# Performance work log

Measured on AMD Instinct MI355X. Metric: run time of the kernel, lower is better.

The kernel has to match this reference:

```python
import jax, jax.numpy as jnp
import numpy as np

B, C, H, W, N = 4, 128, 240, 320, 1024
LEVEL = 8.0          # scaling[0] = 4 * img_scale with img_scale=2
E1_LAMDA = 1.0
E2_LAMDA = 2.0 / 7.0
GN_LAMDA = 0.3
EPS = 1e-9


def extract_features(f, coords):
    # f: (B,C,H,W); coords: (B,N,2) float pixel coords as (x, y)
    Bf, Cf, Hf, Wf = f.shape
    x = coords[..., 0]
    y = coords[..., 1]
    x0 = jnp.floor(x)
    y0 = jnp.floor(y)
    wx = (x - x0)[:, None, :]          # (B,1,N)
    wy = (y - y0)[:, None, :]
    x0i = jnp.clip(x0.astype(jnp.int32), 0, Wf - 1)
    x1i = jnp.clip(x0i + 1, 0, Wf - 1)
    y0i = jnp.clip(y0.astype(jnp.int32), 0, Hf - 1)
    y1i = jnp.clip(y0i + 1, 0, Hf - 1)

    def g(fm, yi, xi):                 # fm: (C,H,W), yi/xi: (N,)
        return fm[:, yi, xi]           # (C,N)

    v00 = jax.vmap(g)(f, y0i, x0i)
    v01 = jax.vmap(g)(f, y0i, x1i)
    v10 = jax.vmap(g)(f, y1i, x0i)
    v11 = jax.vmap(g)(f, y1i, x1i)
    out = (v00 * (1 - wx) * (1 - wy) + v01 * wx * (1 - wy)
           + v10 * (1 - wx) * wy + v11 * wx * wy)          # (B,C,N)
    return out.transpose(0, 2, 1).reshape(Bf * coords.shape[1], Cf)


def l2_normalize(f):
    n = jnp.linalg.norm(f, axis=1, keepdims=True)
    return f / jnp.maximum(n, 1e-12)


def torch_gradient(f):
    # central differences with edge replication; gx = d/dx (width), gy = d/dy (height)
    fpx = jnp.pad(f, ((0, 0), (0, 0), (0, 0), (1, 1)), mode='edge')
    fpy = jnp.pad(f, ((0, 0), (0, 0), (1, 1), (0, 0)), mode='edge')
    gx = 0.5 * (fpx[..., 2:] - fpx[..., :-2])
    gy = 0.5 * (fpy[..., 2:, :] - fpy[..., :-2, :])
    return gx, gy


def compute_gn_loss(f_t, fb, ub, noise):
    Bn, Nn, _ = ub.shape
    xs = (2.0 * noise - 1.0) + ub                   # uniform(-1,1) jitter
    f_s = extract_features(fb, xs)
    f_t = l2_normalize(f_t)
    f_s = l2_normalize(f_s)
    r = f_s - f_t                                   # (BN, C)
    gx, gy = torch_gradient(fb)
    Jx = extract_features(gx, xs)                   # (BN, C)
    Jy = extract_features(gy, xs)
    J = jnp.stack([Jx, Jy], axis=-1)                # (BN, C, 2)
    Hm = jnp.einsum('bci,bcj->bij', J, J) + EPS * jnp.eye(2, dtype=J.dtype)
    b = jnp.einsum('bci,bc->bi', J, r)[..., None]   # (BN, 2, 1)
    # closed-form 2x2 inverse
    a = Hm[:, 0, 0]; bb = Hm[:, 0, 1]; c = Hm[:, 1, 0]; d = Hm[:, 1, 1]
    det = a * d - bb * c
    Hinv = jnp.stack([jnp.stack([d, -bb], -1),
                      jnp.stack([-c, a], -1)], -2) / det[:, None, None]
    miu = xs.reshape(Bn * Nn, 2, 1) - Hinv @ b
    diff = (ub.reshape(Bn * Nn, 2, 1) - miu)[..., 0]          # (BN, 2)
    e1 = 0.5 * jnp.sum(jnp.einsum('bi,bij,bj->b', diff, Hm, diff))
    log_det = jnp.log(det)
    e2 = Bn * Nn * jnp.log(jnp.asarray(2.0 * np.pi, dtype=det.dtype)) - 0.5 * jnp.sum(log_det)
    e = E1_LAMDA * e1 + E2_LAMDA * e2
    return e, e1, e2


def setup_inputs() -> dict:
    key = jax.random.key(0)
    k = jax.random.split(key, 7)
    F_a = jax.random.normal(k[0], (B, C, H, W), dtype=jnp.float32)
    F_b = jax.random.normal(k[1], (B, C, H, W), dtype=jnp.float32)
    # full-resolution match coords, safely inside the map after /LEVEL
    xa = jax.random.uniform(k[2], (B, N)) * (W - 5) * LEVEL + 2 * LEVEL
    ya = jax.random.uniform(k[3], (B, N)) * (H - 5) * LEVEL + 2 * LEVEL
    xb = jax.random.uniform(k[4], (B, N)) * (W - 5) * LEVEL + 2 * LEVEL
    yb = jax.random.uniform(k[5], (B, N)) * (H - 5) * LEVEL + 2 * LEVEL
    matches_a = jnp.stack([xa, ya], axis=-1)
    matches_b = jnp.stack([xb, yb], axis=-1)
    noise = jax.random.uniform(k[6], (B, N, 2), dtype=jnp.float32)
    return {"F_a": F_a, "F_b": F_b, "matches_a": matches_a,
            "matches_b": matches_b, "noise": noise}


def reference(F_a, F_b, matches_a, matches_b, noise):
    f_t = extract_features(F_a, matches_a / LEVEL)
    e, e1, e2 = compute_gn_loss(f_t, F_b, matches_b / LEVEL, noise)
    return GN_LAMDA * e, e1, e2
```

## Files before the change

### kernel.cpp

```cpp
#include <hip/hip_runtime.h>
#include <math.h>

#define B_  4
#define C_  128
#define H_  240
#define W_  320
#define N_  1024
#define NPTS (B_ * N_)
#define HW_ (H_ * W_)
#define NBINS 960

typedef float f4 __attribute__((ext_vector_type(4)));
typedef float f2 __attribute__((ext_vector_type(2)));

__device__ __forceinline__ f4 load4(const float* p) {
    f4 v; __builtin_memcpy(&v, p, 16); return v;
}
__device__ __forceinline__ f2 load2(const float* p) {
    f2 v; __builtin_memcpy(&v, p, 8); return v;
}
__device__ __forceinline__ void store2(float* p, f2 v) {
    __builtin_memcpy(p, &v, 8);
}

__global__ __launch_bounds__(1024) void gn_sort_kernel(
    const float* __restrict__ ma, const float* __restrict__ mb,
    const float* __restrict__ noise,
    int* __restrict__ permA, int* __restrict__ permB)
{
    __shared__ int hist[NBINS];
    __shared__ int cursor[NBINS];

    for (int i = threadIdx.x; i < NBINS; i += 1024) hist[i] = 0;
    __syncthreads();
    int keyB[4];
    #pragma unroll
    for (int k = 0; k < 4; ++k) {
        const int p = threadIdx.x + (k << 10);
        const float ys = 2.0f * noise[p * 2 + 1] - 1.0f + mb[p * 2 + 1] * 0.125f;
        const int y0 = min(max((int)floorf(ys), 1), H_ - 3);
        keyB[k] = (p >> 10) * H_ + y0;
        atomicAdd(&hist[keyB[k]], 1);
    }
    __syncthreads();
    if (threadIdx.x < 64) {
        const int lane = threadIdx.x;
        const int base = lane * 15;
        int loc[15]; int s = 0;
        #pragma unroll
        for (int i = 0; i < 15; ++i) { loc[i] = s; s += hist[base + i]; }
        int incl = s;
        #pragma unroll
        for (int off = 1; off < 64; off <<= 1) {
            const int v = __shfl_up(incl, off, 64);
            if (lane >= off) incl += v;
        }
        const int excl = incl - s;
        #pragma unroll
        for (int i = 0; i < 15; ++i) cursor[base + i] = excl + loc[i];
    }
    __syncthreads();
    #pragma unroll
    for (int k = 0; k < 4; ++k) {
        const int p = threadIdx.x + (k << 10);
        permB[atomicAdd(&cursor[keyB[k]], 1)] = p;
    }
    __syncthreads();

    for (int i = threadIdx.x; i < NBINS; i += 1024) hist[i] = 0;
    __syncthreads();
    int keyA[4];
    #pragma unroll
    for (int k = 0; k < 4; ++k) {
        const int p = threadIdx.x + (k << 10);
        const float ya = ma[p * 2 + 1] * 0.125f;
        const int y0 = min(max((int)floorf(ya), 0), H_ - 2);
        keyA[k] = (p >> 10) * H_ + y0;
        atomicAdd(&hist[keyA[k]], 1);
    }
    __syncthreads();
    if (threadIdx.x < 64) {
        const int lane = threadIdx.x;
        const int base = lane * 15;
        int loc[15]; int s = 0;
        #pragma unroll
        for (int i = 0; i < 15; ++i) { loc[i] = s; s += hist[base + i]; }
        int incl = s;
        #pragma unroll
        for (int off = 1; off < 64; off <<= 1) {
            const int v = __shfl_up(incl, off, 64);
            if (lane >= off) incl += v;
        }
        const int excl = incl - s;
        #pragma unroll
        for (int i = 0; i < 15; ++i) cursor[base + i] = excl + loc[i];
    }
    __syncthreads();
    #pragma unroll
    for (int k = 0; k < 4; ++k) {
        const int p = threadIdx.x + (k << 10);
        permA[atomicAdd(&cursor[keyA[k]], 1)] = p;
    }
}

__global__ __launch_bounds__(256) void gn_ft_kernel(
    const float* __restrict__ Fa, const float* __restrict__ ma,
    const int* __restrict__ permA, float* __restrict__ ws_ft)
{
    const int w    = (blockIdx.x << 2) | (threadIdx.x >> 6);
    const int lane = threadIdx.x & 63;
    const int pg   = w >> 6;
    const int c0   = (w & 63) << 1;
    const int p    = permA[(pg << 6) | lane];
    const int b    = p >> 10;

    const float xa = ma[p * 2 + 0] * 0.125f;
    const float ya = ma[p * 2 + 1] * 0.125f;
    const float ax0f = floorf(xa), ay0f = floorf(ya);
    const float awx = xa - ax0f, awy = ya - ay0f;
    const int ax0 = min(max((int)ax0f, 0), W_ - 2);
    const int ay0 = min(max((int)ay0f, 0), H_ - 2);
    const int o0 = ay0 * W_ + ax0;
    const int o1 = o0 + W_;

    const float* __restrict__ fa0 = Fa + ((size_t)(b * C_ + c0)) * HW_;
    const float* __restrict__ fa1 = fa0 + HW_;

    const f2 a0_0 = load2(fa0 + o0);
    const f2 a1_0 = load2(fa0 + o1);
    const f2 a0_1 = load2(fa1 + o0);
    const f2 a1_1 = load2(fa1 + o1);

    const float w00 = (1.f - awx) * (1.f - awy);
    const float w01 = awx * (1.f - awy);
    const float w10 = (1.f - awx) * awy;
    const float w11 = awx * awy;

    f2 ft;
    ft.x = a0_0.x * w00 + a0_0.y * w01 + a1_0.x * w10 + a1_0.y * w11;
    ft.y = a0_1.x * w00 + a0_1.y * w01 + a1_1.x * w10 + a1_1.y * w11;
    store2(ws_ft + (size_t)p * C_ + c0, ft);
}

__global__ __launch_bounds__(256) void gn_fb_kernel(
    const float* __restrict__ Fb, const float* __restrict__ mb,
    const float* __restrict__ noise, const int* __restrict__ permB,
    float* __restrict__ fjp)
{
    const int w    = (blockIdx.x << 2) | (threadIdx.x >> 6);
    const int lane = threadIdx.x & 63;
    const int pg   = w >> 6;
    const int c0   = (w & 63) << 1;
    const int p    = permB[(pg << 6) | lane];
    const int b    = p >> 10;

    const float ubx = mb[p * 2 + 0] * 0.125f;
    const float uby = mb[p * 2 + 1] * 0.125f;
    const float xs  = 2.0f * noise[p * 2 + 0] - 1.0f + ubx;
    const float ys  = 2.0f * noise[p * 2 + 1] - 1.0f + uby;

    const float bx0f = floorf(xs), by0f = floorf(ys);
    const float wx = xs - bx0f, wy = ys - by0f;
    const int x0 = min(max((int)bx0f, 1), W_ - 3);
    const int y0 = min(max((int)by0f, 1), H_ - 3);

    const int o_y0 = y0 * W_ + (x0 - 1);
    const int o_y1 = o_y0 + W_;
    const int o_ym = (y0 - 1) * W_ + x0;
    const int o_yp = (y0 + 2) * W_ + x0;

    const float* __restrict__ fb0 = Fb + ((size_t)(b * C_ + c0)) * HW_;
    const float* __restrict__ fb1 = fb0 + HW_;

    const f4 r0_0 = load4(fb0 + o_y0);
    const f4 r1_0 = load4(fb0 + o_y1);
    const f2 rm_0 = load2(fb0 + o_ym);
    const f2 rp_0 = load2(fb0 + o_yp);
    const f4 r0_1 = load4(fb1 + o_y0);
    const f4 r1_1 = load4(fb1 + o_y1);
    const f2 rm_1 = load2(fb1 + o_ym);
    const f2 rp_1 = load2(fb1 + o_yp);

    const float w00 = (1.f - wx) * (1.f - wy);
    const float w01 = wx * (1.f - wy);
    const float w10 = (1.f - wx) * wy;
    const float w11 = wx * wy;

    #pragma unroll
    for (int ch = 0; ch < 2; ++ch) {
        const f4 row0 = ch ? r0_1 : r0_0;
        const f4 row1 = ch ? r1_1 : r1_0;
        const f2 rm   = ch ? rm_1 : rm_0;
        const f2 rp   = ch ? rp_1 : rp_0;
        const float fs = row0.y * w00 + row0.z * w01 + row1.y * w10 + row1.z * w11;
        const float jx = 0.5f * ((row0.z - row0.x) * w00 + (row0.w - row0.y) * w01
                               + (row1.z - row1.x) * w10 + (row1.w - row1.y) * w11);
        const float jy = 0.5f * ((row1.y - rm.x) * w00 + (row1.z - rm.y) * w01
                               + (rp.x - row0.y) * w10 + (rp.y - row0.z) * w11);
        const size_t base = (size_t)(c0 + ch) * 3 * NPTS + p;
        fjp[base]            = fs;
        fjp[base + NPTS]     = jx;
        fjp[base + 2 * NPTS] = jy;
    }
}

__global__ __launch_bounds__(256) void gn_combine_kernel(
    const float* __restrict__ ws_ft, const float* __restrict__ fjp,
    const float* __restrict__ mb, const float* __restrict__ noise,
    float* __restrict__ ws_e1, float* __restrict__ ws_ld)
{
    const int p = blockIdx.x * 256 + threadIdx.x;

    float s[9];
    #pragma unroll
    for (int k = 0; k < 9; ++k) s[k] = 0.f;

    const float* ftp = ws_ft + (size_t)p * C_;
    #pragma unroll 4
    for (int c = 0; c < C_; ++c) {
        const float ft = ftp[c];
        const size_t base = (size_t)c * 3 * NPTS + p;
        const float fs = fjp[base];
        const float jx = fjp[base + NPTS];
        const float jy = fjp[base + 2 * NPTS];
        s[0] += ft * ft;
        s[1] += fs * fs;
        s[2] += jx * fs;
        s[3] += jx * ft;
        s[4] += jy * fs;
        s[5] += jy * ft;
        s[6] += jx * jx;
        s[7] += jx * jy;
        s[8] += jy * jy;
    }

    const float ubx = mb[p * 2 + 0] * 0.125f;
    const float uby = mb[p * 2 + 1] * 0.125f;
    const float xs  = 2.0f * noise[p * 2 + 0] - 1.0f + ubx;
    const float ys  = 2.0f * noise[p * 2 + 1] - 1.0f + uby;

    const float nt = fmaxf(sqrtf(s[0]), 1e-12f);
    const float ns = fmaxf(sqrtf(s[1]), 1e-12f);
    const float b0 = s[2] / ns - s[3] / nt;
    const float b1 = s[4] / ns - s[5] / nt;
    const float H00 = s[6] + 1e-9f;
    const float H01 = s[7];
    const float H11 = s[8] + 1e-9f;
    const float det = H00 * H11 - H01 * H01;
    const float inv = 1.0f / det;
    const float u0 = (H11 * b0 - H01 * b1) * inv;
    const float u1 = (H00 * b1 - H01 * b0) * inv;
    const float d0 = (ubx - xs) + u0;
    const float d1 = (uby - ys) + u1;
    const float quad = d0 * (H00 * d0 + H01 * d1) + d1 * (H01 * d0 + H11 * d1);
    ws_e1[p] = 0.5f * quad;
    ws_ld[p] = logf(det);
}

__global__ __launch_bounds__(256) void gn_reduce_kernel(
    const float* __restrict__ ws_e1, const float* __restrict__ ws_ld,
    float* __restrict__ out)
{
    __shared__ double sm1[256];
    __shared__ double sm2[256];
    double a1 = 0.0, a2 = 0.0;
    for (int i = threadIdx.x; i < NPTS; i += 256) {
        a1 += (double)ws_e1[i];
        a2 += (double)ws_ld[i];
    }
    sm1[threadIdx.x] = a1;
    sm2[threadIdx.x] = a2;
    __syncthreads();
    for (int s = 128; s > 0; s >>= 1) {
        if (threadIdx.x < s) {
            sm1[threadIdx.x] += sm1[threadIdx.x + s];
            sm2[threadIdx.x] += sm2[threadIdx.x + s];
        }
        __syncthreads();
    }
    if (threadIdx.x == 0) {
        const double e1 = sm1[0];
        const double sum_ld = sm2[0];
        const double log2pi = (double)logf(6.283185307179586f);
        const double e2 = (double)NPTS * log2pi - 0.5 * sum_ld;
        const double e = 1.0 * e1 + (2.0 / 7.0) * e2;
        out[0] = (float)(0.3 * e);
        out[1] = (float)e1;
        out[2] = (float)e2;
    }
}

extern "C" void kernel_launch(void* const* d_in, const int* in_sizes, int n_in,
                              void* d_out, int out_size, void* d_ws, size_t ws_size,
                              hipStream_t stream) {
    const float* Fa    = (const float*)d_in[0];
    const float* Fb    = (const float*)d_in[1];
    const float* ma    = (const float*)d_in[2];
    const float* mb    = (const float*)d_in[3];
    const float* noise = (const float*)d_in[4];
    float* out = (float*)d_out;

    float* ws_e1 = (float*)d_ws;
    float* ws_ld = ws_e1 + NPTS;
    int*   permA = (int*)(ws_ld + NPTS);
    int*   permB = permA + NPTS;
    float* ws_ft = (float*)(permB + NPTS);
    float* fjp   = ws_ft + (size_t)NPTS * C_;

    gn_sort_kernel<<<1, 1024, 0, stream>>>(ma, mb, noise, permA, permB);
    gn_ft_kernel<<<1024, 256, 0, stream>>>(Fa, ma, permA, ws_ft);
    gn_fb_kernel<<<1024, 256, 0, stream>>>(Fb, mb, noise, permB, fjp);
    gn_combine_kernel<<<NPTS / 256, 256, 0, stream>>>(ws_ft, fjp, mb, noise,
                                                      ws_e1, ws_ld);
    gn_reduce_kernel<<<1, 256, 0, stream>>>(ws_e1, ws_ld, out);
}
```

Before: 74.52 us.

## Stage Fb row slabs in LDS and fuse F_a/F_b gathers into one launch

The F_b gather now has one block per (batch, channel, 30-row slab). Each block loads the slab plus halo rows of the plane into LDS with coalesced vector loads, then serves all points whose bin falls in that slab from shared memory, replacing scattered global loads. The F_a gather moves into the same launch as extra blocks and writes f_t in sorted, channel-major order through an inverse permutation. Combine then reads coalesced in sorted order with 64-thread blocks. This trades scattered reads for streaming whole planes (all of F_b is read) and uses about 42KB of LDS per block, which limits occupancy.

```diff
diff --git a/kernel.cpp b/kernel.cpp
--- a/kernel.cpp
+++ b/kernel.cpp
@@ -9,6 +9,11 @@
 #define NPTS (B_ * N_)
 #define HW_ (H_ * W_)
 #define NBINS 960
+#define SLAB  30
+#define NSLAB 8
+#define LROWS 33
+#define LDSF  (LROWS * W_)
+#define NFB   (B_ * C_ * NSLAB)
 
 typedef float f4 __attribute__((ext_vector_type(4)));
 typedef float f2 __attribute__((ext_vector_type(2)));
@@ -18,15 +23,13 @@
 }
 __device__ __forceinline__ f2 load2(const float* p) {
     f2 v; __builtin_memcpy(&v, p, 8); return v;
-}
-__device__ __forceinline__ void store2(float* p, f2 v) {
-    __builtin_memcpy(p, &v, 8);
 }
 
 __global__ __launch_bounds__(1024) void gn_sort_kernel(
     const float* __restrict__ ma, const float* __restrict__ mb,
     const float* __restrict__ noise,
-    int* __restrict__ permA, int* __restrict__ permB)
+    int* __restrict__ permA, int* __restrict__ permB,
+    int* __restrict__ invB, int* __restrict__ binStart)
 {
     __shared__ int hist[NBINS];
     __shared__ int cursor[NBINS];
@@ -60,10 +63,15 @@
         for (int i = 0; i < 15; ++i) cursor[base + i] = excl + loc[i];
     }
     __syncthreads();
+    for (int i = threadIdx.x; i < NBINS; i += 1024) binStart[i] = cursor[i];
+    if (threadIdx.x == 0) binStart[NBINS] = NPTS;
+    __syncthreads();
     #pragma unroll
     for (int k = 0; k < 4; ++k) {
         const int p = threadIdx.x + (k << 10);
-        permB[atomicAdd(&cursor[keyB[k]], 1)] = p;
+        const int pos = atomicAdd(&cursor[keyB[k]], 1);
+        permB[pos] = p;
+        invB[p] = pos;
     }
     __syncthreads();
 
@@ -103,123 +111,139 @@
     }
 }
 
-__global__ __launch_bounds__(256) void gn_ft_kernel(
-    const float* __restrict__ Fa, const float* __restrict__ ma,
-    const int* __restrict__ permA, float* __restrict__ ws_ft)
+__global__ __launch_bounds__(256) void gn_gather_kernel(
+    const float* __restrict__ Fa, const float* __restrict__ Fb,
+    const float* __restrict__ ma, const float* __restrict__ mb,
+    const float* __restrict__ noise,
+    const int* __restrict__ permA, const int* __restrict__ permB,
+    const int* __restrict__ invB, const int* __restrict__ binStart,
+    float* __restrict__ ws_ft, float* __restrict__ fjp)
 {
-    const int w    = (blockIdx.x << 2) | (threadIdx.x >> 6);
-    const int lane = threadIdx.x & 63;
-    const int pg   = w >> 6;
-    const int c0   = (w & 63) << 1;
-    const int p    = permA[(pg << 6) | lane];
-    const int b    = p >> 10;
-
-    const float xa = ma[p * 2 + 0] * 0.125f;
-    const float ya = ma[p * 2 + 1] * 0.125f;
-    const float ax0f = floorf(xa), ay0f = floorf(ya);
-    const float awx = xa - ax0f, awy = ya - ay0f;
-    const int ax0 = min(max((int)ax0f, 0), W_ - 2);
-    const int ay0 = min(max((int)ay0f, 0), H_ - 2);
-    const int o0 = ay0 * W_ + ax0;
-    const int o1 = o0 + W_;
-
-    const float* __restrict__ fa0 = Fa + ((size_t)(b * C_ + c0)) * HW_;
-    const float* __restrict__ fa1 = fa0 + HW_;
-
-    const f2 a0_0 = load2(fa0 + o0);
-    const f2 a1_0 = load2(fa0 + o1);
-    const f2 a0_1 = load2(fa1 + o0);
-    const f2 a1_1 = load2(fa1 + o1);
-
-    const float w00 = (1.f - awx) * (1.f - awy);
-    const float w01 = awx * (1.f - awy);
-    const float w10 = (1.f - awx) * awy;
-    const float w11 = awx * awy;
-
-    f2 ft;
-    ft.x = a0_0.x * w00 + a0_0.y * w01 + a1_0.x * w10 + a1_0.y * w11;
-    ft.y = a0_1.x * w00 + a0_1.y * w01 + a1_1.x * w10 + a1_1.y * w11;
-    store2(ws_ft + (size_t)p * C_ + c0, ft);
-}
-
-__global__ __launch_bounds__(256) void gn_fb_kernel(
-    const float* __restrict__ Fb, const float* __restrict__ mb,
-    const float* __restrict__ noise, const int* __restrict__ permB,
-    float* __restrict__ fjp)
-{
-    const int w    = (blockIdx.x << 2) | (threadIdx.x >> 6);
-    const int lane = threadIdx.x & 63;
-    const int pg   = w >> 6;
-    const int c0   = (w & 63) << 1;
-    const int p    = permB[(pg << 6) | lane];
-    const int b    = p >> 10;
-
-    const float ubx = mb[p * 2 + 0] * 0.125f;
-    const float uby = mb[p * 2 + 1] * 0.125f;
-    const float xs  = 2.0f * noise[p * 2 + 0] - 1.0f + ubx;
-    const float ys  = 2.0f * noise[p * 2 + 1] - 1.0f + uby;
-
-    const float bx0f = floorf(xs), by0f = floorf(ys);
-    const float wx = xs - bx0f, wy = ys - by0f;
-    const int x0 = min(max((int)bx0f, 1), W_ - 3);
-    const int y0 = min(max((int)by0f, 1), H_ - 3);
-
-    const int o_y0 = y0 * W_ + (x0 - 1);
-    const int o_y1 = o_y0 + W_;
-    const int o_ym = (y0 - 1) * W_ + x0;
-    const int o_yp = (y0 + 2) * W_ + x0;
-
-    const float* __restrict__ fb0 = Fb + ((size_t)(b * C_ + c0)) * HW_;
-    const float* __restrict__ fb1 = fb0 + HW_;
-
-    const f4 r0_0 = load4(fb0 + o_y0);
-    const f4 r1_0 = load4(fb0 + o_y1);
-    const f2 rm_0 = load2(fb0 + o_ym);
-    const f2 rp_0 = load2(fb0 + o_yp);
-    const f4 r0_1 = load4(fb1 + o_y0);
-    const f4 r1_1 = load4(fb1 + o_y1);
-    const f2 rm_1 = load2(fb1 + o_ym);
-    const f2 rp_1 = load2(fb1 + o_yp);
-
-    const float w00 = (1.f - wx) * (1.f - wy);
-    const float w01 = wx * (1.f - wy);
-    const float w10 = (1.f - wx) * wy;
-    const float w11 = wx * wy;
-
-    #pragma unroll
-    for (int ch = 0; ch < 2; ++ch) {
-        const f4 row0 = ch ? r0_1 : r0_0;
-        const f4 row1 = ch ? r1_1 : r1_0;
-        const f2 rm   = ch ? rm_1 : rm_0;
-        const f2 rp   = ch ? rp_1 : rp_0;
-        const float fs = row0.y * w00 + row0.z * w01 + row1.y * w10 + row1.z * w11;
-        const float jx = 0.5f * ((row0.z - row0.x) * w00 + (row0.w - row0.y) * w01
-                               + (row1.z - row1.x) * w10 + (row1.w - row1.y) * w11);
-        const float jy = 0.5f * ((row1.y - rm.x) * w00 + (row1.z - rm.y) * w01
-                               + (rp.x - row0.y) * w10 + (rp.y - row0.z) * w11);
-        const size_t base = (size_t)(c0 + ch) * 3 * NPTS + p;
-        fjp[base]            = fs;
-        fjp[base + NPTS]     = jx;
-        fjp[base + 2 * NPTS] = jy;
-    }
-}
-
-__global__ __launch_bounds__(256) void gn_combine_kernel(
+    __shared__ float rows[LDSF];
+    const int tid = threadIdx.x;
+
+    if (blockIdx.x < NFB) {
+        const int blk = blockIdx.x;
+        const int c  = blk & (C_ - 1);
+        const int bs = blk >> 7;
+        const int b  = bs >> 3;
+        const int s  = bs & (NSLAB - 1);
+        const int ybase = s * SLAB - 1;
+
+        const float* __restrict__ plane = Fb + ((size_t)(b * C_ + c)) * HW_;
+        const int srcbase = ybase * W_;
+
+        for (int i = tid; i < LDSF / 4; i += 256) {
+            const int flat = i << 2;
+            const int src = srcbase + flat;
+            f4 v = {0.f, 0.f, 0.f, 0.f};
+            if (src >= 0 && src < HW_) v = load4(plane + src);
+            *(f4*)&rows[flat] = v;
+        }
+        __syncthreads();
+
+        const int binbase = b * H_ + s * SLAB;
+        const int pLo = binStart[binbase];
+        const int pHi = binStart[binbase + SLAB];
+
+        for (int i = pLo + tid; i < pHi; i += 256) {
+            const int p = permB[i];
+            const float ubx = mb[p * 2 + 0] * 0.125f;
+            const float uby = mb[p * 2 + 1] * 0.125f;
+            const float xs  = 2.0f * noise[p * 2 + 0] - 1.0f + ubx;
+            const float ys  = 2.0f * noise[p * 2 + 1] - 1.0f + uby;
+
+            const float bx0f = floorf(xs), by0f = floorf(ys);
+            const float wx = xs - bx0f, wy = ys - by0f;
+            const int x0 = min(max((int)bx0f, 1), W_ - 3);
+            const int y0 = min(max((int)by0f, 1), H_ - 3);
+            const int rel = y0 - ybase;
+
+            const float* rY0 = &rows[rel * W_];
+            const float* rY1 = rY0 + W_;
+            const float* rYm = rY0 - W_;
+            const float* rYp = rY1 + W_;
+
+            const float r0m = rY0[x0 - 1], r00 = rY0[x0];
+            const float r01 = rY0[x0 + 1], r0p = rY0[x0 + 2];
+            const float r1m = rY1[x0 - 1], r10 = rY1[x0];
+            const float r11 = rY1[x0 + 1], r1p = rY1[x0 + 2];
+            const float rm0 = rYm[x0],     rm1 = rYm[x0 + 1];
+            const float rp0 = rYp[x0],     rp1 = rYp[x0 + 1];
+
+            const float w00 = (1.f - wx) * (1.f - wy);
+            const float w01 = wx * (1.f - wy);
+            const float w10 = (1.f - wx) * wy;
+            const float w11 = wx * wy;
+
+            const float fs = r00 * w00 + r01 * w01 + r10 * w10 + r11 * w11;
+            const float jx = 0.5f * ((r01 - r0m) * w00 + (r0p - r00) * w01
+                                   + (r11 - r1m) * w10 + (r1p - r10) * w11);
+            const float jy = 0.5f * ((r10 - rm0) * w00 + (r11 - rm1) * w01
+                                   + (rp0 - r00) * w10 + (rp1 - r01) * w11);
+
+            const size_t base = (size_t)c * 3 * NPTS + i;
+            fjp[base]            = fs;
+            fjp[base + NPTS]     = jx;
+            fjp[base + 2 * NPTS] = jy;
+        }
+    } else {
+        const int fi   = blockIdx.x - NFB;
+        const int w    = (fi << 2) | (tid >> 6);
+        const int lane = tid & 63;
+        const int pg   = w >> 6;
+        const int c0   = (w & 63) << 1;
+        const int p    = permA[(pg << 6) | lane];
+        const int b    = p >> 10;
+
+        const float xa = ma[p * 2 + 0] * 0.125f;
+        const float ya = ma[p * 2 + 1] * 0.125f;
+        const float ax0f = floorf(xa), ay0f = floorf(ya);
+        const float awx = xa - ax0f, awy = ya - ay0f;
+        const int ax0 = min(max((int)ax0f, 0), W_ - 2);
+        const int ay0 = min(max((int)ay0f, 0), H_ - 2);
+        const int o0 = ay0 * W_ + ax0;
+        const int o1 = o0 + W_;
+
+        const float* __restrict__ fa0 = Fa + ((size_t)(b * C_ + c0)) * HW_;
+        const float* __restrict__ fa1 = fa0 + HW_;
+
+        const f2 a0_0 = load2(fa0 + o0);
+        const f2 a1_0 = load2(fa0 + o1);
+        const f2 a0_1 = load2(fa1 + o0);
+        const f2 a1_1 = load2(fa1 + o1);
+
+        const float w00 = (1.f - awx) * (1.f - awy);
+        const float w01 = awx * (1.f - awy);
+        const float w10 = (1.f - awx) * awy;
+        const float w11 = awx * awy;
+
+        const float ft0 = a0_0.x * w00 + a0_0.y * w01 + a1_0.x * w10 + a1_0.y * w11;
+        const float ft1 = a0_1.x * w00 + a0_1.y * w01 + a1_1.x * w10 + a1_1.y * w11;
+
+        const int slot = invB[p];
+        ws_ft[(size_t)c0 * NPTS + slot]       = ft0;
+        ws_ft[(size_t)(c0 + 1) * NPTS + slot] = ft1;
+    }
+}
+
+__global__ __launch_bounds__(64) void gn_combine_kernel(
     const float* __restrict__ ws_ft, const float* __restrict__ fjp,
     const float* __restrict__ mb, const float* __restrict__ noise,
+    const int* __restrict__ permB,
     float* __restrict__ ws_e1, float* __restrict__ ws_ld)
 {
-    const int p = blockIdx.x * 256 + threadIdx.x;
+    const int i = blockIdx.x * 64 + threadIdx.x;
+    const int p = permB[i];
 
     float s[9];
     #pragma unroll
     for (int k = 0; k < 9; ++k) s[k] = 0.f;
 
-    const float* ftp = ws_ft + (size_t)p * C_;
     #pragma unroll 4
     for (int c = 0; c < C_; ++c) {
-        const float ft = ftp[c];
-        const size_t base = (size_t)c * 3 * NPTS + p;
+        const float ft = ws_ft[(size_t)c * NPTS + i];
+        const size_t base = (size_t)c * 3 * NPTS + i;
         const float fs = fjp[base];
         const float jx = fjp[base + NPTS];
         const float jy = fjp[base + 2 * NPTS];
@@ -300,17 +324,21 @@
     const float* noise = (const float*)d_in[4];
     float* out = (float*)d_out;
 
-    float* ws_e1 = (float*)d_ws;
-    float* ws_ld = ws_e1 + NPTS;
-    int*   permA = (int*)(ws_ld + NPTS);
-    int*   permB = permA + NPTS;
-    float* ws_ft = (float*)(permB + NPTS);
-    float* fjp   = ws_ft + (size_t)NPTS * C_;
-
-    gn_sort_kernel<<<1, 1024, 0, stream>>>(ma, mb, noise, permA, permB);
-    gn_ft_kernel<<<1024, 256, 0, stream>>>(Fa, ma, permA, ws_ft);
-    gn_fb_kernel<<<1024, 256, 0, stream>>>(Fb, mb, noise, permB, fjp);
-    gn_combine_kernel<<<NPTS / 256, 256, 0, stream>>>(ws_ft, fjp, mb, noise,
-                                                      ws_e1, ws_ld);
+    float* ws_e1    = (float*)d_ws;
+    float* ws_ld    = ws_e1 + NPTS;
+    int*   permA    = (int*)(ws_ld + NPTS);
+    int*   permB    = permA + NPTS;
+    int*   invB     = permB + NPTS;
+    int*   binStart = invB + NPTS;
+    float* ws_ft    = (float*)(binStart + 1024);
+    float* fjp      = ws_ft + (size_t)C_ * NPTS;
+
+    gn_sort_kernel<<<1, 1024, 0, stream>>>(ma, mb, noise, permA, permB,
+                                           invB, binStart);
+    gn_gather_kernel<<<NFB + 1024, 256, 0, stream>>>(Fa, Fb, ma, mb, noise,
+                                                     permA, permB, invB,
+                                                     binStart, ws_ft, fjp);
+    gn_combine_kernel<<<NPTS / 64, 64, 0, stream>>>(ws_ft, fjp, mb, noise,
+                                                    permB, ws_e1, ws_ld);
     gn_reduce_kernel<<<1, 256, 0, stream>>>(ws_e1, ws_ld, out);
 }
```

New measurement: 89.59 us. +20.2%, slower.
